# Optimization experiments

Hardware: AMD Instinct MI355X
Metric: run time of the kernel (lower is better)

Reference implementation:

```python
import jax, jax.numpy as jnp
import numpy as np

N = 100000; E = 1600000; C = 32; H = 2
KS = (3, 3, 5, 5)
NEG = 0.01      # LeakyReLU default slope
GAT_NEG = 0.2   # SuperGAT attention leaky_relu slope
EPS = 1e-5      # BatchNorm eps


def setup_inputs() -> dict:
    key = jax.random.key(0)
    ks = jax.random.split(key, 64)
    inp = {}
    inp["patch_embs"] = jax.random.normal(ks[0], (N, C), dtype=jnp.float32)
    ei = np.array(jax.random.randint(ks[1], (2, E), 0, N))
    # avoid self loops so PyG's remove_self_loops/add_self_loops semantics match exactly
    ei[1] = np.where(ei[0] == ei[1], (ei[1] + 1) % N, ei[1])
    inp["edge_index"] = jnp.array(ei, dtype=jnp.int32)
    inp["edge_attr"] = jax.random.normal(ks[2], (E, 1), dtype=jnp.float32)
    s = 1.0 / np.sqrt(C)
    i = 3
    for b in range(4):
        inp[f"W{b}"] = (jax.random.normal(ks[i], (KS[b], C, C)) * s).astype(jnp.float32); i += 1
        inp[f"cb{b}"] = jnp.zeros((C,), jnp.float32)                     # ChebConv bias
        inp[f"G{b}"] = (jax.random.normal(ks[i], (C, H * C)) * s).astype(jnp.float32); i += 1  # SuperGAT lin
        inp[f"al{b}"] = (jax.random.normal(ks[i], (H, C)) * s).astype(jnp.float32); i += 1     # att_l
        inp[f"ar{b}"] = (jax.random.normal(ks[i], (H, C)) * s).astype(jnp.float32); i += 1     # att_r
        inp[f"gb{b}"] = jnp.zeros((C,), jnp.float32)                     # SuperGAT bias
        inp[f"gm{b}"] = jnp.ones((C,), jnp.float32)                      # BN gamma
        inp[f"bt{b}"] = jnp.zeros((C,), jnp.float32)                     # BN beta
    return inp


def _cheb(x, src, dst, w, W, cb):
    # ChebConv with sym Laplacian, lambda_max=2 -> L_hat = -D^-1/2 A D^-1/2
    def spmv(v):
        return jax.ops.segment_sum(w[:, None] * v[src], dst, num_segments=N)
    tx0, out = x, x @ W[0]
    tx1 = spmv(x)
    out = out + tx1 @ W[1]
    for k in range(2, W.shape[0]):
        tx0, tx1 = tx1, 2.0 * spmv(tx1) - tx0
        out = out + tx1 @ W[k]
    return out + cb


def _supergat(x, ssrc, sdst, G, al, ar, gb):
    # SuperGATConv, attention_type='MX', heads=2, concat=False (mean)
    h = (x @ G).reshape(N, H, C)          # [N,H,C]
    hi, hj = h[sdst], h[ssrc]              # gathered per edge (incl. self loops)
    logits = jnp.sum(hi * hj, -1)          # [Etot,H]
    a = jnp.sum(hj * al, -1) + jnp.sum(hi * ar, -1)
    a = jax.nn.leaky_relu(a * jax.nn.sigmoid(logits), GAT_NEG)
    amax = jax.ops.segment_max(a, sdst, num_segments=N)
    ex = jnp.exp(a - amax[sdst])
    den = jax.ops.segment_sum(ex, sdst, num_segments=N)
    alpha = ex / (den[sdst] + 1e-16)
    out = jax.ops.segment_sum(alpha[..., None] * hj, sdst, num_segments=N)
    return out.mean(axis=1) + gb


def _block(x, src, dst, w, ssrc, sdst, W, cb, G, al, ar, gb, gm, bt):
    s_ = _supergat(_cheb(x, src, dst, w, W, cb), ssrc, sdst, G, al, ar, gb)
    y = jax.nn.leaky_relu(s_, NEG) + s_
    mu = y.mean(0)
    var = y.var(0)  # biased var, matches torch BN training normalization
    return gm * (y - mu) / jnp.sqrt(var + EPS) + bt


def _forward(x, edge_index, params):
    src, dst = edge_index[0], edge_index[1]
    deg = jax.ops.segment_sum(jnp.ones((E,), jnp.float32), src, num_segments=N)
    di = deg[src] * deg[dst]
    w = jnp.where(di > 0, -1.0 / jnp.sqrt(jnp.maximum(di, 1e-12)), 0.0)
    loop = jnp.arange(N, dtype=edge_index.dtype)
    ssrc = jnp.concatenate([src, loop])
    sdst = jnp.concatenate([dst, loop])
    acc = 0.0
    for b in range(4):
        W, cb, G, al, ar, gb, gm, bt = params[b]
        acc = acc + _block(x, src, dst, w, ssrc, sdst, W, cb, G, al, ar, gb, gm, bt)
    return jax.nn.leaky_relu(acc, NEG)


def reference(patch_embs, edge_index, edge_attr,
              W0, cb0, G0, al0, ar0, gb0, gm0, bt0,
              W1, cb1, G1, al1, ar1, gb1, gm1, bt1,
              W2, cb2, G2, al2, ar2, gb2, gm2, bt2,
              W3, cb3, G3, al3, ar3, gb3, gm3, bt3):
    params = [(W0, cb0, G0, al0, ar0, gb0, gm0, bt0),
              (W1, cb1, G1, al1, ar1, gb1, gm1, bt1),
              (W2, cb2, G2, al2, ar2, gb2, gm2, bt2),
              (W3, cb3, G3, al3, ar3, gb3, gm3, bt3)]
    return _forward(patch_embs, edge_index, params)
```

## Files before the change

### kernel.cpp

```cpp
#include <hip/hip_runtime.h>
#include <math.h>

#define NN 100000
#define EE 1600000
#define CCH 32
#define NC (NN*CCH)
#define ET (EE+NN)
#define NEGS 0.01f
#define GNEG 0.2f
#define BEPS 1e-5f

#define DSWZ(x, pat) __int_as_float(__builtin_amdgcn_ds_swizzle(__float_as_int(x), pat))
#define RED32(v) do{ v += DSWZ(v,0x041F); v += DSWZ(v,0x081F); v += DSWZ(v,0x101F); \
                     v += DSWZ(v,0x201F); v += DSWZ(v,0x401F); }while(0)


__global__ void k_degs(const int* __restrict__ src, const int* __restrict__ dst,
                       float* __restrict__ deg_out, int* __restrict__ indeg){
    int e = blockIdx.x*blockDim.x + threadIdx.x;
    if (e >= EE) return;
    atomicAdd(&deg_out[src[e]], 1.0f);
    atomicAdd(&indeg[dst[e]], 1);
}

#define SCAN_T 1024
__global__ void k_scan(const int* __restrict__ indeg, int* __restrict__ row){
    __shared__ int sdata[SCAN_T];
    int t = threadIdx.x;
    const int per = (NN + SCAN_T - 1)/SCAN_T;
    int lo = t*per, hi = (lo + per < NN) ? lo + per : NN;
    int s = 0;
    for (int d = lo; d < hi; d++) s += indeg[d] + 1;
    sdata[t] = s;
    __syncthreads();
    for (int off = 1; off < SCAN_T; off <<= 1){
        int v = (t >= off) ? sdata[t-off] : 0;
        __syncthreads();
        sdata[t] += v;
        __syncthreads();
    }
    int excl = (t == 0) ? 0 : sdata[t-1];
    for (int d = lo; d < hi; d++){
        row[d] = excl;
        excl += indeg[d] + 1;
    }
    if (t == 0) row[NN] = ET;
}

__global__ void k_self(const int* __restrict__ row, int* __restrict__ csr_srcb,
                       float* __restrict__ csr_w){
    int d = blockIdx.x*blockDim.x + threadIdx.x;
    if (d >= NN) return;
    int p = row[d];
    csr_srcb[p] = d << 7;
    csr_w[p] = 0.0f;
}

__global__ void k_scatter(const int* __restrict__ src, const int* __restrict__ dst,
                          const float* __restrict__ deg_out, const int* __restrict__ row,
                          int* __restrict__ cur, int* __restrict__ csr_srcb,
                          float* __restrict__ csr_w){
    int e = blockIdx.x*blockDim.x + threadIdx.x;
    if (e >= EE) return;
    int s = src[e], d = dst[e];
    int pos = row[d] + 1 + atomicAdd(&cur[d], 1);
    csr_srcb[pos] = s << 7;
    float di = deg_out[s] * deg_out[d];
    csr_w[pos] = (di > 0.0f) ? (-__frsqrt_rn(fmaxf(di, 1e-12f))) : 0.0f;
}

__global__ void k_spmv_csr(const int* __restrict__ row, const int* __restrict__ csr_srcb,
                           const float* __restrict__ csr_w, const float* __restrict__ v,
                           const float* __restrict__ tprev, float* __restrict__ out, int first){
    int gid = blockIdx.x*blockDim.x + threadIdx.x;
    int node = gid >> 6;
    if (node >= NN) return;
    int lane = gid & 63;
    int slot = lane >> 4;
    int l = lane & 15;
    const char* vb = (const char*)v + (l << 3);
    int start = row[node] + 1, end = row[node+1];
    float2 acc = {0.0f, 0.0f};
    int p = start + slot;
    for (; p + 12 < end; p += 16){
        int b0 = csr_srcb[p], b1 = csr_srcb[p+4], b2 = csr_srcb[p+8], b3 = csr_srcb[p+12];
        float w0 = csr_w[p], w1 = csr_w[p+4], w2 = csr_w[p+8], w3 = csr_w[p+12];
        float2 v0 = *(const float2*)(vb + (size_t)(unsigned)b0);
        float2 v1 = *(const float2*)(vb + (size_t)(unsigned)b1);
        float2 v2 = *(const float2*)(vb + (size_t)(unsigned)b2);
        float2 v3 = *(const float2*)(vb + (size_t)(unsigned)b3);
        acc.x += w0*v0.x + w1*v1.x + w2*v2.x + w3*v3.x;
        acc.y += w0*v0.y + w1*v1.y + w2*v2.y + w3*v3.y;
    }
    for (; p < end; p += 4){
        float w0 = csr_w[p];
        float2 v0 = *(const float2*)(vb + (size_t)(unsigned)csr_srcb[p]);
        acc.x += w0*v0.x;
        acc.y += w0*v0.y;
    }
    acc.x += __shfl_xor(acc.x, 32); acc.y += __shfl_xor(acc.y, 32);
    acc.x += DSWZ(acc.x, 0x401F);  acc.y += DSWZ(acc.y, 0x401F);
    if (slot == 0){
        float2 r;
        if (first){
            r = acc;
        } else {
            float2 t = ((const float2*)tprev)[(size_t)node*16 + l];
            r.x = 2.0f*acc.x - t.x;
            r.y = 2.0f*acc.y - t.y;
        }
        ((float2*)out)[(size_t)node*16 + l] = r;
    }
}

__global__ void k_wg(const float* __restrict__ W, const float* __restrict__ cb,
                     const float* __restrict__ G, float* __restrict__ Wg,
                     float* __restrict__ cbg, int K){
    int t = blockIdx.x*blockDim.x + threadIdx.x;
    if (t < K*2048){
        int k = t >> 11, r = t & 2047;
        int i = r >> 6, j = r & 63;
        float s = 0.0f;
        #pragma unroll 8
        for (int q = 0; q < 32; q++) s += W[k*1024 + i*32 + q] * G[q*64 + j];
        Wg[t] = s;
    } else if (t < K*2048 + 64){
        int j = t - K*2048;
        float s = 0.0f;
        #pragma unroll 8
        for (int q = 0; q < 32; q++) s += cb[q] * G[q*64 + j];
        cbg[j] = s;
    }
}

__global__ void k_hfused(const float* __restrict__ T0, const float* __restrict__ T1,
                         const float* __restrict__ T2, const float* __restrict__ T3,
                         const float* __restrict__ T4,
                         const float* __restrict__ Wg, const float* __restrict__ cbg,
                         const float* __restrict__ al, const float* __restrict__ ar,
                         int K, int b, float* __restrict__ H4,
                         float* __restrict__ attL4, float* __restrict__ attR4){
    __shared__ float sW[5*2048];
    for (int i = threadIdx.x; i < K*2048; i += blockDim.x) sW[i] = Wg[i];
    __syncthreads();
    int gid = blockIdx.x*blockDim.x + threadIdx.x;
    int node = gid >> 6;
    if (node >= NN) return;
    int lane = gid & 63;
    int h = lane >> 5, c = lane & 31;
    const float* Ts[5] = {T0, T1, T2, T3, T4};
    float acc = cbg[lane];
    for (int k = 0; k < K; k++){
        float tv = Ts[k][(size_t)node*CCH + c];
        const float* wrow = &sW[k*2048];
        #pragma unroll
        for (int i = 0; i < 32; i++){
            float t = __shfl(tv, i);
            acc += t * wrow[i*64 + lane];
        }
    }
    H4[(size_t)node*256 + lane*4 + b] = acc;
    float va = acc * al[lane];
    float vr = acc * ar[lane];
    RED32(va);
    RED32(vr);
    if (c == 0){
        attL4[(size_t)node*8 + h*4 + b] = va;
        attR4[(size_t)node*8 + h*4 + b] = vr;
    }
}

__global__ __launch_bounds__(512)
void k_gat4(const int* __restrict__ row, const int* __restrict__ csr_srcb,
            const float* __restrict__ H4,
            const float* __restrict__ attL4, const float* __restrict__ attR4,
            const float* __restrict__ gb0, const float* __restrict__ gb1,
            const float* __restrict__ gb2, const float* __restrict__ gb3,
            float* __restrict__ y4, float* __restrict__ sums){
    int gid = blockIdx.x*blockDim.x + threadIdx.x;
    int node = gid >> 6;
    int lane = gid & 63;
    int wv_ = threadIdx.x >> 6;
    int h = lane >> 5, c = lane & 31;
    const char* Hb = (const char*)H4 + (lane << 4);
    const char* Lb = (const char*)attL4 + (h << 4);
    __shared__ float4 ssum[8*32], ssq[8*32];
    float4 yv = {0.0f, 0.0f, 0.0f, 0.0f};
    if (node < NN){
        float hiA[4], aiA[4], mA[4], denA[4], accA[4];
        {
            float4 t = *(const float4*)&H4[(size_t)node*256 + lane*4];
            hiA[0]=t.x; hiA[1]=t.y; hiA[2]=t.z; hiA[3]=t.w;
            float4 u = *(const float4*)&attR4[(size_t)node*8 + h*4];
            aiA[0]=u.x; aiA[1]=u.y; aiA[2]=u.z; aiA[3]=u.w;
        }
        #pragma unroll
        for (int k = 0; k < 4; k++){ mA[k] = -1e30f; denA[k] = 0.0f; accA[k] = 0.0f; }
        int start = row[node], end = row[node+1];
        int p = start;
        for (; p + 3 < end; p += 4){
            int sb[4]; float hj[4][4], aL[4][4], lg[4][4];
            #pragma unroll
            for (int i = 0; i < 4; i++) sb[i] = csr_srcb[p+i];
            #pragma unroll
            for (int i = 0; i < 4; i++){
                float4 t = *(const float4*)(Hb + ((size_t)(unsigned)sb[i] << 3));
                hj[i][0]=t.x; hj[i][1]=t.y; hj[i][2]=t.z; hj[i][3]=t.w;
                float4 u = *(const float4*)(Lb + (size_t)(unsigned)(sb[i] >> 2));
                aL[i][0]=u.x; aL[i][1]=u.y; aL[i][2]=u.z; aL[i][3]=u.w;
            }
            #pragma unroll
            for (int i = 0; i < 4; i++)
                #pragma unroll
                for (int k = 0; k < 4; k++) lg[i][k] = hiA[k]*hj[i][k];
            #pragma unroll
            for (int i = 0; i < 4; i++)
                #pragma unroll
                for (int k = 0; k < 4; k++) RED32(lg[i][k]);
            #pragma unroll
            for (int k = 0; k < 4; k++){
                float a0 = (aL[0][k] + aiA[k]) * __builtin_amdgcn_rcpf(1.0f + __expf(-lg[0][k]));
                float a1 = (aL[1][k] + aiA[k]) * __builtin_amdgcn_rcpf(1.0f + __expf(-lg[1][k]));
                float a2 = (aL[2][k] + aiA[k]) * __builtin_amdgcn_rcpf(1.0f + __expf(-lg[2][k]));
                float a3 = (aL[3][k] + aiA[k]) * __builtin_amdgcn_rcpf(1.0f + __expf(-lg[3][k]));
                a0 = fmaxf(a0, GNEG*a0);
                a1 = fmaxf(a1, GNEG*a1);
                a2 = fmaxf(a2, GNEG*a2);
                a3 = fmaxf(a3, GNEG*a3);
                float mn = fmaxf(fmaxf(mA[k], fmaxf(a0, a1)), fmaxf(a2, a3));
                float sc = __expf(mA[k] - mn);
                float w0 = __expf(a0 - mn), w1 = __expf(a1 - mn);
                float w2 = __expf(a2 - mn), w3 = __expf(a3 - mn);
                denA[k] = denA[k]*sc + ((w0 + w1) + (w2 + w3));
                accA[k] = accA[k]*sc + (w0*hj[0][k] + w1*hj[1][k]) + (w2*hj[2][k] + w3*hj[3][k]);
                mA[k] = mn;
            }
        }
        for (; p < end; p++){
            int sb0 = csr_srcb[p];
            float hj0[4], aL0[4], lg0[4];
            float4 t = *(const float4*)(Hb + ((size_t)(unsigned)sb0 << 3));
            hj0[0]=t.x; hj0[1]=t.y; hj0[2]=t.z; hj0[3]=t.w;
            float4 u = *(const float4*)(Lb + (size_t)(unsigned)(sb0 >> 2));
            aL0[0]=u.x; aL0[1]=u.y; aL0[2]=u.z; aL0[3]=u.w;
            #pragma unroll
            for (int k = 0; k < 4; k++) lg0[k] = hiA[k]*hj0[k];
            #pragma unroll
            for (int k = 0; k < 4; k++) RED32(lg0[k]);
            #pragma unroll
            for (int k = 0; k < 4; k++){
                float a0 = (aL0[k] + aiA[k]) * __builtin_amdgcn_rcpf(1.0f + __expf(-lg0[k]));
                a0 = fmaxf(a0, GNEG*a0);
                float mn = fmaxf(mA[k], a0);
                float sc = __expf(mA[k] - mn);
                float w0 = __expf(a0 - mn);
                denA[k] = denA[k]*sc + w0;
                accA[k] = accA[k]*sc + w0*hj0[k];
                mA[k] = mn;
            }
        }
        float g[4];
        g[0] = gb0[c]; g[1] = gb1[c]; g[2] = gb2[c]; g[3] = gb3[c];
        float yo[4];
        #pragma unroll
        for (int k = 0; k < 4; k++){
            float accn = accA[k] * __builtin_amdgcn_rcpf(denA[k] + 1e-16f);
            float s_ = 0.5f*(accn + __shfl_xor(accn, 32)) + g[k];
            yo[k] = (s_ > 0.0f) ? 2.0f*s_ : (1.0f + NEGS)*s_;
        }
        yv.x = yo[0]; yv.y = yo[1]; yv.z = yo[2]; yv.w = yo[3];
        if (h == 0) *(float4*)&y4[(size_t)node*128 + c*4] = yv;
    }
    if (h == 0){
        ssum[wv_*32 + c] = yv;
        float4 q = {yv.x*yv.x, yv.y*yv.y, yv.z*yv.z, yv.w*yv.w};
        ssq[wv_*32 + c] = q;
    }
    __syncthreads();
    if (threadIdx.x < 32){
        float4 s = {0,0,0,0}, q = {0,0,0,0};
        #pragma unroll
        for (int r = 0; r < 8; r++){
            float4 a = ssum[r*32 + threadIdx.x];
            float4 b = ssq[r*32 + threadIdx.x];
            s.x += a.x; s.y += a.y; s.z += a.z; s.w += a.w;
            q.x += b.x; q.y += b.y; q.z += b.z; q.w += b.w;
        }
        atomicAdd(&sums[  0 + threadIdx.x], s.x);
        atomicAdd(&sums[ 32 + threadIdx.x], s.y);
        atomicAdd(&sums[ 64 + threadIdx.x], s.z);
        atomicAdd(&sums[ 96 + threadIdx.x], s.w);
        atomicAdd(&sums[128 + threadIdx.x], q.x);
        atomicAdd(&sums[160 + threadIdx.x], q.y);
        atomicAdd(&sums[192 + threadIdx.x], q.z);
        atomicAdd(&sums[224 + threadIdx.x], q.w);
    }
}

__global__ void k_norm4(const float* __restrict__ y4, const float* __restrict__ sums,
                        const float* __restrict__ gm0, const float* __restrict__ bt0,
                        const float* __restrict__ gm1, const float* __restrict__ bt1,
                        const float* __restrict__ gm2, const float* __restrict__ bt2,
                        const float* __restrict__ gm3, const float* __restrict__ bt3,
                        float* __restrict__ out){
    int t = blockIdx.x*blockDim.x + threadIdx.x;
    if (t >= NC) return;
    int c = t & 31;
    const float invN = 1.0f / (float)NN;
    float4 v = *(const float4*)&y4[(size_t)t*4];
    float r = 0.0f;
    {
        float mu = sums[c]*invN;       float var = sums[128+c]*invN - mu*mu;
        r += gm0[c]*(v.x - mu)/sqrtf(var + BEPS) + bt0[c];
    }
    {
        float mu = sums[32+c]*invN;    float var = sums[160+c]*invN - mu*mu;
        r += gm1[c]*(v.y - mu)/sqrtf(var + BEPS) + bt1[c];
    }
    {
        float mu = sums[64+c]*invN;    float var = sums[192+c]*invN - mu*mu;
        r += gm2[c]*(v.z - mu)/sqrtf(var + BEPS) + bt2[c];
    }
    {
        float mu = sums[96+c]*invN;    float var = sums[224+c]*invN - mu*mu;
        r += gm3[c]*(v.w - mu)/sqrtf(var + BEPS) + bt3[c];
    }
    out[t] = (r > 0.0f) ? r : NEGS*r;
}

extern "C" void kernel_launch(void* const* d_in, const int* in_sizes, int n_in,
                              void* d_out, int out_size, void* d_ws, size_t ws_size,
                              hipStream_t stream){
    const float* x   = (const float*)d_in[0];
    const int*   ei  = (const int*)d_in[1];
    const int*   src = ei;
    const int*   dst = ei + EE;

    const float *Wp[4], *cbp[4], *Gp[4], *alp[4], *arp[4], *gbp[4], *gmp[4], *btp[4];
    for (int b = 0; b < 4; b++){
        int base = 3 + 8*b;
        Wp[b]  = (const float*)d_in[base+0];
        cbp[b] = (const float*)d_in[base+1];
        Gp[b]  = (const float*)d_in[base+2];
        alp[b] = (const float*)d_in[base+3];
        arp[b] = (const float*)d_in[base+4];
        gbp[b] = (const float*)d_in[base+5];
        gmp[b] = (const float*)d_in[base+6];
        btp[b] = (const float*)d_in[base+7];
    }

    char* w8 = (char*)d_ws;
    #define CARVE(ptr_t, name, bytes) ptr_t name = (ptr_t)w8; w8 += (((size_t)(bytes)) + 15) & ~(size_t)15;
    CARVE(float*, deg_out, sizeof(float)*NN)
    CARVE(int*,   indeg,   sizeof(int)*NN)
    CARVE(int*,   cur,     sizeof(int)*NN)
    CARVE(int*,   row,     sizeof(int)*(NN+1))
    CARVE(int*,   csr_srcb, sizeof(int)*ET)
    CARVE(float*, csr_w,   sizeof(float)*ET)
    CARVE(float*, T1,      sizeof(float)*NC)
    CARVE(float*, T2,      sizeof(float)*NC)
    CARVE(float*, T3,      sizeof(float)*NC)
    CARVE(float*, T4,      sizeof(float)*NC)
    CARVE(float*, H4,      sizeof(float)*(size_t)NN*256)
    CARVE(float*, attL4,   sizeof(float)*NN*8)
    CARVE(float*, attR4,   sizeof(float)*NN*8)
    CARVE(float*, Wg,      sizeof(float)*4*5*2048)
    CARVE(float*, cbg,     sizeof(float)*4*64)
    CARVE(float*, sums,    sizeof(float)*256)
    float* y4 = T1;

    float* acc = (float*)d_out;

    const int B = 256;
    const int gE  = (EE + B - 1)/B;
    const int gN  = (NN + B - 1)/B;
    const int gNC = (NC + B - 1)/B;
    const int gW5 = (NN*64 + 511)/512;

    hipMemsetAsync(deg_out, 0, (size_t)3*NN*sizeof(int), stream);
    k_degs<<<gE, B, 0, stream>>>(src, dst, deg_out, indeg);
    k_scan<<<1, SCAN_T, 0, stream>>>(indeg, row);
    k_self<<<gN, B, 0, stream>>>(row, csr_srcb, csr_w);
    k_scatter<<<gE, B, 0, stream>>>(src, dst, deg_out, row, cur, csr_srcb, csr_w);

    k_spmv_csr<<<gW5, 512, 0, stream>>>(row, csr_srcb, csr_w, x,  (const float*)0, T1, 1);
    k_spmv_csr<<<gW5, 512, 0, stream>>>(row, csr_srcb, csr_w, T1, x,  T2, 0);
    k_spmv_csr<<<gW5, 512, 0, stream>>>(row, csr_srcb, csr_w, T2, T1, T3, 0);
    k_spmv_csr<<<gW5, 512, 0, stream>>>(row, csr_srcb, csr_w, T3, T2, T4, 0);

    const int Ks[4] = {3, 3, 5, 5};
    for (int b = 0; b < 4; b++){
        int tot = Ks[b]*2048 + 64;
        k_wg<<<(tot + B - 1)/B, B, 0, stream>>>(Wp[b], cbp[b], Gp[b],
                                                Wg + b*5*2048, cbg + b*64, Ks[b]);
    }

    for (int b = 0; b < 4; b++){
        k_hfused<<<gW5, 512, 0, stream>>>(x, T1, T2, T3, T4, Wg + b*5*2048, cbg + b*64,
                                          alp[b], arp[b], Ks[b], b, H4, attL4, attR4);
    }

    hipMemsetAsync(sums, 0, 256*sizeof(float), stream);
    k_gat4<<<gW5, 512, 0, stream>>>(row, csr_srcb, H4, attL4, attR4,
                                    gbp[0], gbp[1], gbp[2], gbp[3], y4, sums);

    k_norm4<<<gNC, B, 0, stream>>>(y4, sums,
                                   gmp[0], btp[0], gmp[1], btp[1],
                                   gmp[2], btp[2], gmp[3], btp[3], acc);
}
```

Measured before the change: 2.105 ms.

## Relayout H4 block-major so GAT lanes own contiguous channels, cutting reductions

Measured after the change: 4.040 ms. 1.92x slower.

```diff
diff --git a/kernel.cpp b/kernel.cpp
--- a/kernel.cpp
+++ b/kernel.cpp
@@ -13,6 +13,7 @@
 #define DSWZ(x, pat) __int_as_float(__builtin_amdgcn_ds_swizzle(__float_as_int(x), pat))
 #define RED32(v) do{ v += DSWZ(v,0x041F); v += DSWZ(v,0x081F); v += DSWZ(v,0x101F); \
                      v += DSWZ(v,0x201F); v += DSWZ(v,0x401F); }while(0)
+#define RED8(v)  do{ v += DSWZ(v,0x041F); v += DSWZ(v,0x081F); v += DSWZ(v,0x101F); }while(0)
 
 
 __global__ void k_degs(const int* __restrict__ src, const int* __restrict__ dst,
@@ -131,6 +132,14 @@
         for (int q = 0; q < 32; q++) s += cb[q] * G[q*64 + j];
         cbg[j] = s;
     }
+}
+
+__global__ void k_pack(const float* __restrict__ g0, const float* __restrict__ g1,
+                       const float* __restrict__ g2, const float* __restrict__ g3,
+                       float* __restrict__ gbAll){
+    int t = threadIdx.x;
+    const float* gs[4] = {g0, g1, g2, g3};
+    gbAll[t] = gs[t >> 5][t & 31];
 }
 
 __global__ void k_hfused(const float* __restrict__ T0, const float* __restrict__ T1,
@@ -159,7 +168,7 @@
             acc += t * wrow[i*64 + lane];
         }
     }
-    H4[(size_t)node*256 + lane*4 + b] = acc;
+    H4[(size_t)node*256 + b*64 + lane] = acc;
     float va = acc * al[lane];
     float vr = acc * ar[lane];
     RED32(va);
@@ -174,107 +183,96 @@
 void k_gat4(const int* __restrict__ row, const int* __restrict__ csr_srcb,
             const float* __restrict__ H4,
             const float* __restrict__ attL4, const float* __restrict__ attR4,
-            const float* __restrict__ gb0, const float* __restrict__ gb1,
-            const float* __restrict__ gb2, const float* __restrict__ gb3,
-            float* __restrict__ y4, float* __restrict__ sums){
+            const float* __restrict__ gbAll,
+            float* __restrict__ y4b, float* __restrict__ sums){
     int gid = blockIdx.x*blockDim.x + threadIdx.x;
     int node = gid >> 6;
     int lane = gid & 63;
     int wv_ = threadIdx.x >> 6;
-    int h = lane >> 5, c = lane & 31;
-    const char* Hb = (const char*)H4 + (lane << 4);
-    const char* Lb = (const char*)attL4 + (h << 4);
+    int bb = lane >> 4, hh = (lane >> 3) & 1, c4 = lane & 7;
+    const char* Hb = (const char*)H4 + ((size_t)lane << 4);
+    const char* Lb = (const char*)attL4 + ((size_t)(hh*4 + bb) << 2);
     __shared__ float4 ssum[8*32], ssq[8*32];
     float4 yv = {0.0f, 0.0f, 0.0f, 0.0f};
     if (node < NN){
-        float hiA[4], aiA[4], mA[4], denA[4], accA[4];
-        {
-            float4 t = *(const float4*)&H4[(size_t)node*256 + lane*4];
-            hiA[0]=t.x; hiA[1]=t.y; hiA[2]=t.z; hiA[3]=t.w;
-            float4 u = *(const float4*)&attR4[(size_t)node*8 + h*4];
-            aiA[0]=u.x; aiA[1]=u.y; aiA[2]=u.z; aiA[3]=u.w;
-        }
-        #pragma unroll
-        for (int k = 0; k < 4; k++){ mA[k] = -1e30f; denA[k] = 0.0f; accA[k] = 0.0f; }
+        float4 hi = *(const float4*)&H4[(size_t)node*256 + lane*4];
+        float ai = attR4[(size_t)node*8 + hh*4 + bb];
+        float m = -1e30f, den = 0.0f;
+        float4 acc = {0.0f, 0.0f, 0.0f, 0.0f};
         int start = row[node], end = row[node+1];
         int p = start;
         for (; p + 3 < end; p += 4){
-            int sb[4]; float hj[4][4], aL[4][4], lg[4][4];
-            #pragma unroll
-            for (int i = 0; i < 4; i++) sb[i] = csr_srcb[p+i];
-            #pragma unroll
-            for (int i = 0; i < 4; i++){
-                float4 t = *(const float4*)(Hb + ((size_t)(unsigned)sb[i] << 3));
-                hj[i][0]=t.x; hj[i][1]=t.y; hj[i][2]=t.z; hj[i][3]=t.w;
-                float4 u = *(const float4*)(Lb + (size_t)(unsigned)(sb[i] >> 2));
-                aL[i][0]=u.x; aL[i][1]=u.y; aL[i][2]=u.z; aL[i][3]=u.w;
-            }
-            #pragma unroll
-            for (int i = 0; i < 4; i++)
-                #pragma unroll
-                for (int k = 0; k < 4; k++) lg[i][k] = hiA[k]*hj[i][k];
-            #pragma unroll
-            for (int i = 0; i < 4; i++)
-                #pragma unroll
-                for (int k = 0; k < 4; k++) RED32(lg[i][k]);
-            #pragma unroll
-            for (int k = 0; k < 4; k++){
-                float a0 = (aL[0][k] + aiA[k]) * __builtin_amdgcn_rcpf(1.0f + __expf(-lg[0][k]));
-                float a1 = (aL[1][k] + aiA[k]) * __builtin_amdgcn_rcpf(1.0f + __expf(-lg[1][k]));
-                float a2 = (aL[2][k] + aiA[k]) * __builtin_amdgcn_rcpf(1.0f + __expf(-lg[2][k]));
-                float a3 = (aL[3][k] + aiA[k]) * __builtin_amdgcn_rcpf(1.0f + __expf(-lg[3][k]));
-                a0 = fmaxf(a0, GNEG*a0);
-                a1 = fmaxf(a1, GNEG*a1);
-                a2 = fmaxf(a2, GNEG*a2);
-                a3 = fmaxf(a3, GNEG*a3);
-                float mn = fmaxf(fmaxf(mA[k], fmaxf(a0, a1)), fmaxf(a2, a3));
-                float sc = __expf(mA[k] - mn);
-                float w0 = __expf(a0 - mn), w1 = __expf(a1 - mn);
-                float w2 = __expf(a2 - mn), w3 = __expf(a3 - mn);
-                denA[k] = denA[k]*sc + ((w0 + w1) + (w2 + w3));
-                accA[k] = accA[k]*sc + (w0*hj[0][k] + w1*hj[1][k]) + (w2*hj[2][k] + w3*hj[3][k]);
-                mA[k] = mn;
-            }
+            int sb0 = csr_srcb[p],   sb1 = csr_srcb[p+1];
+            int sb2 = csr_srcb[p+2], sb3 = csr_srcb[p+3];
+            float4 hj0 = *(const float4*)(Hb + ((size_t)(unsigned)sb0 << 3));
+            float4 hj1 = *(const float4*)(Hb + ((size_t)(unsigned)sb1 << 3));
+            float4 hj2 = *(const float4*)(Hb + ((size_t)(unsigned)sb2 << 3));
+            float4 hj3 = *(const float4*)(Hb + ((size_t)(unsigned)sb3 << 3));
+            float aL0 = *(const float*)(Lb + (size_t)(unsigned)(sb0 >> 2));
+            float aL1 = *(const float*)(Lb + (size_t)(unsigned)(sb1 >> 2));
+            float aL2 = *(const float*)(Lb + (size_t)(unsigned)(sb2 >> 2));
+            float aL3 = *(const float*)(Lb + (size_t)(unsigned)(sb3 >> 2));
+            float lg0 = hi.x*hj0.x + hi.y*hj0.y + hi.z*hj0.z + hi.w*hj0.w;
+            float lg1 = hi.x*hj1.x + hi.y*hj1.y + hi.z*hj1.z + hi.w*hj1.w;
+            float lg2 = hi.x*hj2.x + hi.y*hj2.y + hi.z*hj2.z + hi.w*hj2.w;
+            float lg3 = hi.x*hj3.x + hi.y*hj3.y + hi.z*hj3.z + hi.w*hj3.w;
+            RED8(lg0); RED8(lg1); RED8(lg2); RED8(lg3);
+            float a0 = (aL0 + ai) * __builtin_amdgcn_rcpf(1.0f + __expf(-lg0));
+            float a1 = (aL1 + ai) * __builtin_amdgcn_rcpf(1.0f + __expf(-lg1));
+            float a2 = (aL2 + ai) * __builtin_amdgcn_rcpf(1.0f + __expf(-lg2));
+            float a3 = (aL3 + ai) * __builtin_amdgcn_rcpf(1.0f + __expf(-lg3));
+            a0 = fmaxf(a0, GNEG*a0);
+            a1 = fmaxf(a1, GNEG*a1);
+            a2 = fmaxf(a2, GNEG*a2);
+            a3 = fmaxf(a3, GNEG*a3);
+            float mn = fmaxf(fmaxf(m, fmaxf(a0, a1)), fmaxf(a2, a3));
+            float sc = __expf(m - mn);
+            float w0 = __expf(a0 - mn), w1 = __expf(a1 - mn);
+            float w2 = __expf(a2 - mn), w3 = __expf(a3 - mn);
+            den = den*sc + ((w0 + w1) + (w2 + w3));
+            acc.x = acc.x*sc + (w0*hj0.x + w1*hj1.x) + (w2*hj2.x + w3*hj3.x);
+            acc.y = acc.y*sc + (w0*hj0.y + w1*hj1.y) + (w2*hj2.y + w3*hj3.y);
+            acc.z = acc.z*sc + (w0*hj0.z + w1*hj1.z) + (w2*hj2.z + w3*hj3.z);
+            acc.w = acc.w*sc + (w0*hj0.w + w1*hj1.w) + (w2*hj2.w + w3*hj3.w);
+            m = mn;
         }
         for (; p < end; p++){
             int sb0 = csr_srcb[p];
-            float hj0[4], aL0[4], lg0[4];
-            float4 t = *(const float4*)(Hb + ((size_t)(unsigned)sb0 << 3));
-            hj0[0]=t.x; hj0[1]=t.y; hj0[2]=t.z; hj0[3]=t.w;
-            float4 u = *(const float4*)(Lb + (size_t)(unsigned)(sb0 >> 2));
-            aL0[0]=u.x; aL0[1]=u.y; aL0[2]=u.z; aL0[3]=u.w;
-            #pragma unroll
-            for (int k = 0; k < 4; k++) lg0[k] = hiA[k]*hj0[k];
-            #pragma unroll
-            for (int k = 0; k < 4; k++) RED32(lg0[k]);
-            #pragma unroll
-            for (int k = 0; k < 4; k++){
-                float a0 = (aL0[k] + aiA[k]) * __builtin_amdgcn_rcpf(1.0f + __expf(-lg0[k]));
-                a0 = fmaxf(a0, GNEG*a0);
-                float mn = fmaxf(mA[k], a0);
-                float sc = __expf(mA[k] - mn);
-                float w0 = __expf(a0 - mn);
-                denA[k] = denA[k]*sc + w0;
-                accA[k] = accA[k]*sc + w0*hj0[k];
-                mA[k] = mn;
-            }
+            float4 hj0 = *(const float4*)(Hb + ((size_t)(unsigned)sb0 << 3));
+            float aL0 = *(const float*)(Lb + (size_t)(unsigned)(sb0 >> 2));
+            float lg0 = hi.x*hj0.x + hi.y*hj0.y + hi.z*hj0.z + hi.w*hj0.w;
+            RED8(lg0);
+            float a0 = (aL0 + ai) * __builtin_amdgcn_rcpf(1.0f + __expf(-lg0));
+            a0 = fmaxf(a0, GNEG*a0);
+            float mn = fmaxf(m, a0);
+            float sc = __expf(m - mn);
+            float w0 = __expf(a0 - mn);
+            den = den*sc + w0;
+            acc.x = acc.x*sc + w0*hj0.x;
+            acc.y = acc.y*sc + w0*hj0.y;
+            acc.z = acc.z*sc + w0*hj0.z;
+            acc.w = acc.w*sc + w0*hj0.w;
+            m = mn;
         }
-        float g[4];
-        g[0] = gb0[c]; g[1] = gb1[c]; g[2] = gb2[c]; g[3] = gb3[c];
-        float yo[4];
-        #pragma unroll
-        for (int k = 0; k < 4; k++){
-            float accn = accA[k] * __builtin_amdgcn_rcpf(denA[k] + 1e-16f);
-            float s_ = 0.5f*(accn + __shfl_xor(accn, 32)) + g[k];
-            yo[k] = (s_ > 0.0f) ? 2.0f*s_ : (1.0f + NEGS)*s_;
-        }
-        yv.x = yo[0]; yv.y = yo[1]; yv.z = yo[2]; yv.w = yo[3];
-        if (h == 0) *(float4*)&y4[(size_t)node*128 + c*4] = yv;
-    }
-    if (h == 0){
-        ssum[wv_*32 + c] = yv;
+        float idn = __builtin_amdgcn_rcpf(den + 1e-16f);
+        float4 an = {acc.x*idn, acc.y*idn, acc.z*idn, acc.w*idn};
+        float4 ot = {DSWZ(an.x, 0x201F), DSWZ(an.y, 0x201F),
+                     DSWZ(an.z, 0x201F), DSWZ(an.w, 0x201F)};
+        float4 g = *(const float4*)&gbAll[bb*32 + c4*4];
+        float sx = 0.5f*(an.x + ot.x) + g.x;
+        float sy = 0.5f*(an.y + ot.y) + g.y;
+        float sz = 0.5f*(an.z + ot.z) + g.z;
+        float sw = 0.5f*(an.w + ot.w) + g.w;
+        yv.x = fmaxf(2.0f*sx, (1.0f + NEGS)*sx);
+        yv.y = fmaxf(2.0f*sy, (1.0f + NEGS)*sy);
+        yv.z = fmaxf(2.0f*sz, (1.0f + NEGS)*sz);
+        yv.w = fmaxf(2.0f*sw, (1.0f + NEGS)*sw);
+        if (hh == 0) *(float4*)&y4b[(size_t)bb*NC + (size_t)node*32 + c4*4] = yv;
+    }
+    if (hh == 0){
+        ssum[wv_*32 + bb*8 + c4] = yv;
         float4 q = {yv.x*yv.x, yv.y*yv.y, yv.z*yv.z, yv.w*yv.w};
-        ssq[wv_*32 + c] = q;
+        ssq[wv_*32 + bb*8 + c4] = q;
     }
     __syncthreads();
     if (threadIdx.x < 32){
@@ -286,18 +284,19 @@
             s.x += a.x; s.y += a.y; s.z += a.z; s.w += a.w;
             q.x += b.x; q.y += b.y; q.z += b.z; q.w += b.w;
         }
-        atomicAdd(&sums[  0 + threadIdx.x], s.x);
-        atomicAdd(&sums[ 32 + threadIdx.x], s.y);
-        atomicAdd(&sums[ 64 + threadIdx.x], s.z);
-        atomicAdd(&sums[ 96 + threadIdx.x], s.w);
-        atomicAdd(&sums[128 + threadIdx.x], q.x);
-        atomicAdd(&sums[160 + threadIdx.x], q.y);
-        atomicAdd(&sums[192 + threadIdx.x], q.z);
-        atomicAdd(&sums[224 + threadIdx.x], q.w);
-    }
-}
-
-__global__ void k_norm4(const float* __restrict__ y4, const float* __restrict__ sums,
+        int bo = (threadIdx.x >> 3)*32 + (threadIdx.x & 7)*4;
+        atomicAdd(&sums[bo + 0], s.x);
+        atomicAdd(&sums[bo + 1], s.y);
+        atomicAdd(&sums[bo + 2], s.z);
+        atomicAdd(&sums[bo + 3], s.w);
+        atomicAdd(&sums[128 + bo + 0], q.x);
+        atomicAdd(&sums[128 + bo + 1], q.y);
+        atomicAdd(&sums[128 + bo + 2], q.z);
+        atomicAdd(&sums[128 + bo + 3], q.w);
+    }
+}
+
+__global__ void k_norm4(const float* __restrict__ y4b, const float* __restrict__ sums,
                         const float* __restrict__ gm0, const float* __restrict__ bt0,
                         const float* __restrict__ gm1, const float* __restrict__ bt1,
                         const float* __restrict__ gm2, const float* __restrict__ bt2,
@@ -307,23 +306,26 @@
     if (t >= NC) return;
     int c = t & 31;
     const float invN = 1.0f / (float)NN;
-    float4 v = *(const float4*)&y4[(size_t)t*4];
     float r = 0.0f;
     {
+        float v = y4b[t];
         float mu = sums[c]*invN;       float var = sums[128+c]*invN - mu*mu;
-        r += gm0[c]*(v.x - mu)/sqrtf(var + BEPS) + bt0[c];
+        r += gm0[c]*(v - mu)/sqrtf(var + BEPS) + bt0[c];
     }
     {
+        float v = y4b[NC + t];
         float mu = sums[32+c]*invN;    float var = sums[160+c]*invN - mu*mu;
-        r += gm1[c]*(v.y - mu)/sqrtf(var + BEPS) + bt1[c];
+        r += gm1[c]*(v - mu)/sqrtf(var + BEPS) + bt1[c];
     }
     {
+        float v = y4b[2*NC + t];
         float mu = sums[64+c]*invN;    float var = sums[192+c]*invN - mu*mu;
-        r += gm2[c]*(v.z - mu)/sqrtf(var + BEPS) + bt2[c];
+        r += gm2[c]*(v - mu)/sqrtf(var + BEPS) + bt2[c];
     }
     {
+        float v = y4b[3*NC + t];
         float mu = sums[96+c]*invN;    float var = sums[224+c]*invN - mu*mu;
-        r += gm3[c]*(v.w - mu)/sqrtf(var + BEPS) + bt3[c];
+        r += gm3[c]*(v - mu)/sqrtf(var + BEPS) + bt3[c];
     }
     out[t] = (r > 0.0f) ? r : NEGS*r;
 }
@@ -367,7 +369,8 @@
     CARVE(float*, Wg,      sizeof(float)*4*5*2048)
     CARVE(float*, cbg,     sizeof(float)*4*64)
     CARVE(float*, sums,    sizeof(float)*256)
-    float* y4 = T1;
+    CARVE(float*, gbAll,   sizeof(float)*128)
+    float* y4b = T1;
 
     float* acc = (float*)d_out;
 
@@ -394,6 +397,7 @@
         k_wg<<<(tot + B - 1)/B, B, 0, stream>>>(Wp[b], cbp[b], Gp[b],
                                                 Wg + b*5*2048, cbg + b*64, Ks[b]);
     }
+    k_pack<<<1, 128, 0, stream>>>(gbp[0], gbp[1], gbp[2], gbp[3], gbAll);
 
     for (int b = 0; b < 4; b++){
         k_hfused<<<gW5, 512, 0, stream>>>(x, T1, T2, T3, T4, Wg + b*5*2048, cbg + b*64,
@@ -401,10 +405,9 @@
     }
 
     hipMemsetAsync(sums, 0, 256*sizeof(float), stream);
-    k_gat4<<<gW5, 512, 0, stream>>>(row, csr_srcb, H4, attL4, attR4,
-                                    gbp[0], gbp[1], gbp[2], gbp[3], y4, sums);
-
-    k_norm4<<<gNC, B, 0, stream>>>(y4, sums,
+    k_gat4<<<gW5, 512, 0, stream>>>(row, csr_srcb, H4, attL4, attR4, gbAll, y4b, sums);
+
+    k_norm4<<<gNC, B, 0, stream>>>(y4b, sums,
                                    gmp[0], btp[0], gmp[1], btp[1],
                                    gmp[2], btp[2], gmp[3], btp[3], acc);
 }
```
